# Kernel tuning notes

Hardware: AMD Instinct MI355X
Metric: run time of the kernel (lower is better)

## Reference

```python
import jax, jax.numpy as jnp
import numpy as np

FEATURE_DIM = 1024
HEAD_NUM = 16
HIDDEN_DIM = FEATURE_DIM // HEAD_NUM


def setup_inputs() -> dict:
    key = jax.random.key(0)
    ks = jax.random.split(key, 12)
    B, S, D = 4, 2048, FEATURE_DIM
    s = 1.0 / np.sqrt(D)
    inp = {
        "query": jax.random.normal(ks[0], (B, S, D), jnp.float32),
        "key": jax.random.normal(ks[1], (B, S, D), jnp.float32),
        "value": jax.random.normal(ks[2], (B, S, D), jnp.float32),
        "mask": jax.random.randint(ks[3], (B, 1, 1, S), 0, 2, jnp.int32),
        "Wq": jax.random.normal(ks[4], (D, D), jnp.float32) * s,
        "bq": jnp.zeros((D,), jnp.float32),
        "Wk": jax.random.normal(ks[5], (D, D), jnp.float32) * s,
        "bk": jnp.zeros((D,), jnp.float32),
        "Wv": jax.random.normal(ks[6], (D, D), jnp.float32) * s,
        "bv": jnp.zeros((D,), jnp.float32),
        "Wo": jax.random.normal(ks[7], (D, D), jnp.float32) * s,
        "bo": jnp.zeros((D,), jnp.float32),
    }
    return inp


def reference(query, key, value, mask, Wq, bq, Wk, bk, Wv, bv, Wo, bo):
    B, Sq, D = query.shape
    H, Hd = HEAD_NUM, HIDDEN_DIM
    scale = jnp.sqrt(jnp.asarray(Hd, query.dtype))

    def split_heads(x):
        b, s, _ = x.shape
        return x.reshape(b, s, H, Hd).transpose(0, 2, 1, 3)  # [B,H,S,Hd]

    Q = split_heads(query @ Wq.T + bq)
    K = split_heads(key @ Wk.T + bk)
    V = split_heads(value @ Wv.T + bv)

    scores = jnp.einsum("bhqd,bhkd->bhqk", Q, K) / scale
    scores = jnp.where(mask == 0, jnp.asarray(-1e10, scores.dtype), scores)
    attn = jax.nn.softmax(scores, axis=-1)  # dropout p=0 -> identity
    h = jnp.einsum("bhqk,bhkd->bhqd", attn, V)
    h = h.transpose(0, 2, 1, 3).reshape(B, Sq, D)
    return h @ Wo.T + bo
```

## Files before the change

kernel.cpp:

```cpp
#include <hip/hip_runtime.h>
#include <hip/hip_bf16.h>
#include <cstdint>
#include <cstddef>

#define D_MODEL 1024
#define SEQ     2048
#define BATCH   4
#define NHEAD   16
#define HD      64
#define MROWS   (BATCH * SEQ)

typedef __attribute__((ext_vector_type(8))) short  short8;
typedef __attribute__((ext_vector_type(4))) float  floatx4;
typedef __attribute__((ext_vector_type(4))) unsigned short ushort4v;
typedef unsigned short u16;

__device__ __forceinline__ u16 f2bf(float x) {
    __hip_bfloat16 h = __float2bfloat16(x);
    return *(u16*)&h;
}

__device__ __forceinline__ void async_copy16(const u16* g, u16* l) {
    __builtin_amdgcn_global_load_lds(
        (const __attribute__((address_space(1))) void*)g,
        (__attribute__((address_space(3))) void*)l, 16, 0, 0);
}

__device__ __forceinline__ void cvt8(const float* s, u16* d, size_t i) {
    const float4 a = *(const float4*)(s + i);
    const float4 b = *(const float4*)(s + i + 4);
    short8 o;
    o[0] = (short)f2bf(a.x); o[1] = (short)f2bf(a.y);
    o[2] = (short)f2bf(a.z); o[3] = (short)f2bf(a.w);
    o[4] = (short)f2bf(b.x); o[5] = (short)f2bf(b.y);
    o[6] = (short)f2bf(b.z); o[7] = (short)f2bf(b.w);
    *(short8*)(d + i) = o;
}

__global__ __launch_bounds__(256) void cvt7(
    const float* __restrict__ s0, const float* __restrict__ s1,
    const float* __restrict__ s2, const float* __restrict__ s3,
    const float* __restrict__ s4, const float* __restrict__ s5,
    const float* __restrict__ s6,
    u16* __restrict__ d0, u16* __restrict__ d1,
    u16* __restrict__ d2, u16* __restrict__ d3,
    u16* __restrict__ d4, u16* __restrict__ d5,
    u16* __restrict__ d6)
{
    const int y = blockIdx.y;
    const float* s;
    u16* d;
    size_t n;
    switch (y) {
        case 0: s = s0; d = d0; n = (size_t)D_MODEL * D_MODEL; break;
        case 1: s = s1; d = d1; n = (size_t)D_MODEL * D_MODEL; break;
        case 2: s = s2; d = d2; n = (size_t)D_MODEL * D_MODEL; break;
        case 3: s = s3; d = d3; n = (size_t)D_MODEL * D_MODEL; break;
        case 4: s = s4; d = d4; n = (size_t)MROWS * D_MODEL;   break;
        case 5: s = s5; d = d5; n = (size_t)MROWS * D_MODEL;   break;
        default: s = s6; d = d6; n = (size_t)MROWS * D_MODEL;  break;
    }
    const size_t i = ((size_t)blockIdx.x * 256 + threadIdx.x) * 8;
    if (i < n) cvt8(s, d, i);
}

__global__ __launch_bounds__(256) void gemm_qkv(
    const u16* __restrict__ Aq, const u16* __restrict__ Ak,
    const u16* __restrict__ Av,
    const u16* __restrict__ Wqp, const u16* __restrict__ Wkp,
    const u16* __restrict__ Wvp,
    const float* __restrict__ bqp, const float* __restrict__ bkp,
    const float* __restrict__ bvp,
    u16* __restrict__ oq, u16* __restrict__ ok, u16* __restrict__ ov)
{
    constexpr int K = D_MODEL;
    __shared__ __align__(16) u16 smem[32768];

    const int z = blockIdx.z;
    const u16*   A    = z == 0 ? Aq  : (z == 1 ? Ak  : Av);
    const u16*   W    = z == 0 ? Wqp : (z == 1 ? Wkp : Wvp);
    const float* bias = z == 0 ? bqp : (z == 1 ? bkp : bvp);
    u16*         out  = z == 0 ? oq  : (z == 1 ? ok  : ov);

    const int bm = blockIdx.x * 128;
    const int bn = blockIdx.y * 128;
    const int t  = threadIdx.x;
    const int w  = t >> 6;
    const int l  = t & 63;
    const int li = l & 15;
    const int quad = l >> 4;
    const int wm = (w & 1) * 64;
    const int wn = (w >> 1) * 64;
    const int lrow = l >> 3;
    const int lcol = (l & 7) * 8;

    const u16* Ag = A + (size_t)bm * K;
    const u16* Wg = W + (size_t)bn * K;

    floatx4 acc[4][4];
    #pragma unroll
    for (int mi = 0; mi < 4; mi++)
        #pragma unroll
        for (int ni = 0; ni < 4; ni++) acc[mi][ni] = (floatx4){0.f,0.f,0.f,0.f};

    #pragma unroll
    for (int j = 0; j < 4; j++) {
        const int r = w * 32 + j * 8;
        async_copy16(Ag + (size_t)(r + lrow) * K + lcol, smem + r * 64);
        async_copy16(Wg + (size_t)(r + lrow) * K + lcol, smem + 8192 + r * 64);
    }

    int cur = 0;
    for (int kt = 0; kt < K; kt += 64) {
        __syncthreads();

        if (kt + 64 < K) {
            u16* Asn = smem + (cur ^ 1) * 16384;
            u16* Wsn = Asn + 8192;
            #pragma unroll
            for (int j = 0; j < 4; j++) {
                const int r = w * 32 + j * 8;
                async_copy16(Ag + (size_t)(r + lrow) * K + kt + 64 + lcol, Asn + r * 64);
                async_copy16(Wg + (size_t)(r + lrow) * K + kt + 64 + lcol, Wsn + r * 64);
            }
        }

        const u16* Asc = smem + cur * 16384;
        const u16* Wsc = Asc + 8192;
        #pragma unroll
        for (int ks = 0; ks < 2; ks++) {
            short8 af[4], bf[4];
            #pragma unroll
            for (int i = 0; i < 4; i++) {
                af[i] = *(const short8*)&Asc[(wm + i * 16 + li) * 64 + ks * 32 + quad * 8];
                bf[i] = *(const short8*)&Wsc[(wn + i * 16 + li) * 64 + ks * 32 + quad * 8];
            }
            #pragma unroll
            for (int mi = 0; mi < 4; mi++)
                #pragma unroll
                for (int ni = 0; ni < 4; ni++)
                    acc[mi][ni] = __builtin_amdgcn_mfma_f32_16x16x32_bf16(
                        af[mi], bf[ni], acc[mi][ni], 0, 0, 0);
        }
        cur ^= 1;
    }

    if (z < 2) {
        #pragma unroll
        for (int mi = 0; mi < 4; mi++)
            #pragma unroll
            for (int ni = 0; ni < 4; ni++) {
                const int c  = bn + wn + ni * 16 + li;
                const int h  = c >> 6;
                const int hd = c & 63;
                const float bz = bias[c];
                #pragma unroll
                for (int reg = 0; reg < 4; reg++) {
                    const int r = bm + wm + mi * 16 + quad * 4 + reg;
                    const int b = r >> 11;
                    const int s = r & (SEQ - 1);
                    out[(((size_t)(b * NHEAD + h) * SEQ) + s) * HD + hd] = f2bf(acc[mi][ni][reg] + bz);
                }
            }
    } else {
        u16 (*Ct)[128] = (u16(*)[128])smem;
        __syncthreads();
        #pragma unroll
        for (int mi = 0; mi < 4; mi++)
            #pragma unroll
            for (int ni = 0; ni < 4; ni++) {
                const int cl = wn + ni * 16 + li;
                const float bz = bias[bn + cl];
                #pragma unroll
                for (int reg = 0; reg < 4; reg++) {
                    const int rl = wm + mi * 16 + quad * 4 + reg;
                    Ct[cl][rl] = f2bf(acc[mi][ni][reg] + bz);
                }
            }
        __syncthreads();
        const int cl   = t >> 1;
        const int half = t & 1;
        const int cg = bn + cl;
        const int h  = cg >> 6;
        const int hd = cg & 63;
        const int b  = bm >> 11;
        const int s0 = (bm & (SEQ - 1)) + half * 64;
        u16* dst = out + (((size_t)(b * NHEAD + h) * HD) + hd) * SEQ + s0;
        const short8* sp = (const short8*)&Ct[cl][half * 64];
        #pragma unroll
        for (int i = 0; i < 8; i++) ((short8*)dst)[i] = sp[i];
    }
}

__global__ __launch_bounds__(256) void gemm_out(
    const u16* __restrict__ A,
    const u16* __restrict__ W,
    const float* __restrict__ bias,
    float* __restrict__ out)
{
    constexpr int K = D_MODEL;
    __shared__ __align__(16) u16 smem[32768];

    const int bm = blockIdx.x * 128;
    const int bn = blockIdx.y * 128;
    const int t  = threadIdx.x;
    const int w  = t >> 6;
    const int l  = t & 63;
    const int li = l & 15;
    const int quad = l >> 4;
    const int wm = (w & 1) * 64;
    const int wn = (w >> 1) * 64;
    const int lrow = l >> 3;
    const int lcol = (l & 7) * 8;

    const u16* Ag = A + (size_t)bm * K;
    const u16* Wg = W + (size_t)bn * K;

    floatx4 acc[4][4];
    #pragma unroll
    for (int mi = 0; mi < 4; mi++)
        #pragma unroll
        for (int ni = 0; ni < 4; ni++) acc[mi][ni] = (floatx4){0.f,0.f,0.f,0.f};

    #pragma unroll
    for (int j = 0; j < 4; j++) {
        const int r = w * 32 + j * 8;
        async_copy16(Ag + (size_t)(r + lrow) * K + lcol, smem + r * 64);
        async_copy16(Wg + (size_t)(r + lrow) * K + lcol, smem + 8192 + r * 64);
    }

    int cur = 0;
    for (int kt = 0; kt < K; kt += 64) {
        __syncthreads();

        if (kt + 64 < K) {
            u16* Asn = smem + (cur ^ 1) * 16384;
            u16* Wsn = Asn + 8192;
            #pragma unroll
            for (int j = 0; j < 4; j++) {
                const int r = w * 32 + j * 8;
                async_copy16(Ag + (size_t)(r + lrow) * K + kt + 64 + lcol, Asn + r * 64);
                async_copy16(Wg + (size_t)(r + lrow) * K + kt + 64 + lcol, Wsn + r * 64);
            }
        }

        const u16* Asc = smem + cur * 16384;
        const u16* Wsc = Asc + 8192;
        #pragma unroll
        for (int ks = 0; ks < 2; ks++) {
            short8 af[4], bf[4];
            #pragma unroll
            for (int i = 0; i < 4; i++) {
                af[i] = *(const short8*)&Asc[(wm + i * 16 + li) * 64 + ks * 32 + quad * 8];
                bf[i] = *(const short8*)&Wsc[(wn + i * 16 + li) * 64 + ks * 32 + quad * 8];
            }
            #pragma unroll
            for (int mi = 0; mi < 4; mi++)
                #pragma unroll
                for (int ni = 0; ni < 4; ni++)
                    acc[mi][ni] = __builtin_amdgcn_mfma_f32_16x16x32_bf16(
                        af[mi], bf[ni], acc[mi][ni], 0, 0, 0);
        }
        cur ^= 1;
    }

    #pragma unroll
    for (int mi = 0; mi < 4; mi++)
        #pragma unroll
        for (int ni = 0; ni < 4; ni++) {
            const int c = bn + wn + ni * 16 + li;
            const float bz = bias[c];
            #pragma unroll
            for (int reg = 0; reg < 4; reg++) {
                const int r = bm + wm + mi * 16 + quad * 4 + reg;
                out[(size_t)r * D_MODEL + c] = acc[mi][ni][reg] + bz;
            }
        }
}

#define LOG2E   1.44269504088896340736f
#define CSCALE  (0.125f * LOG2E)

__global__ __launch_bounds__(256, 4) void attn_mfma(
    const u16* __restrict__ Q,
    const u16* __restrict__ K,
    const u16* __restrict__ Vt,
    const int* __restrict__ mask,
    u16* __restrict__ H)
{
    __shared__ __align__(16) u16 Ks[64 * 64];
    __shared__ __align__(16) u16 Vs[64 * 64];
    __shared__ __align__(16) u16 Ps[4][32][72];
    __shared__ __align__(16) float mc[64];

    const int bh  = blockIdx.y;
    const int b   = bh >> 4;
    const int h   = bh & 15;
    const int q0  = blockIdx.x * 128;
    const int t   = threadIdx.x;
    const int w   = t >> 6;
    const int l   = t & 63;
    const int li  = l & 15;
    const int quad  = l >> 4;
    const int lrow8 = l >> 3;
    const int gch   = (l & 7) ^ lrow8;
    const int swz   = li & 7;

    short8 qf[2][2];
    #pragma unroll
    for (int qb = 0; qb < 2; qb++) {
        const u16* Qrow = Q + ((size_t)bh * SEQ + q0 + w * 32 + qb * 16 + li) * HD;
        qf[qb][0] = *(const short8*)(Qrow + quad * 8);
        qf[qb][1] = *(const short8*)(Qrow + 32 + quad * 8);
    }

    const u16* Kbh = K  + (size_t)bh * SEQ * HD;
    const u16* Vbh = Vt + (size_t)bh * HD * SEQ;
    const int* mg  = mask + (size_t)b * SEQ;

    floatx4 oacc[4][2];
    #pragma unroll
    for (int hm = 0; hm < 4; hm++)
        #pragma unroll
        for (int qb = 0; qb < 2; qb++) oacc[hm][qb] = (floatx4){0.f,0.f,0.f,0.f};
    float rs[2] = {0.f, 0.f};

    #pragma unroll
    for (int j = 0; j < 2; j++) {
        const int rb = w * 16 + j * 8;
        async_copy16(Kbh + (size_t)(rb + lrow8) * HD + gch * 8, &Ks[rb * 64]);
    }
    if (t < 64) mc[t] = (mg[t] != 0) ? -16.0f : -1.0e9f;

    for (int kt = 0; kt < SEQ; kt += 64) {
        __syncthreads();

        #pragma unroll
        for (int j = 0; j < 2; j++) {
            const int rb = w * 16 + j * 8;
            async_copy16(Vbh + (size_t)(rb + lrow8) * SEQ + kt + gch * 8,
                         &Vs[rb * 64]);
        }

        #pragma unroll
        for (int kb = 0; kb < 4; kb++) {
            floatx4 s0 = (floatx4){0.f,0.f,0.f,0.f};
            floatx4 s1 = (floatx4){0.f,0.f,0.f,0.f};
            #pragma unroll
            for (int ks = 0; ks < 2; ks++) {
                const short8 kf = *(const short8*)
                    &Ks[(kb * 16 + li) * 64 + ((ks * 4 + quad) ^ swz) * 8];
                __builtin_amdgcn_s_setprio(1);
                s0 = __builtin_amdgcn_mfma_f32_16x16x32_bf16(kf, qf[0][ks], s0, 0, 0, 0);
                s1 = __builtin_amdgcn_mfma_f32_16x16x32_bf16(kf, qf[1][ks], s1, 0, 0, 0);
                __builtin_amdgcn_s_setprio(0);
            }
            const float4 m4 = *(const float4*)&mc[kb * 16 + quad * 4];
            {
                const float p0 = __builtin_amdgcn_exp2f(fmaf(s0[0], CSCALE, m4.x));
                const float p1 = __builtin_amdgcn_exp2f(fmaf(s0[1], CSCALE, m4.y));
                const float p2 = __builtin_amdgcn_exp2f(fmaf(s0[2], CSCALE, m4.z));
                const float p3 = __builtin_amdgcn_exp2f(fmaf(s0[3], CSCALE, m4.w));
                rs[0] += (p0 + p1) + (p2 + p3);
                ushort4v pk;
                pk[0] = f2bf(p0); pk[1] = f2bf(p1);
                pk[2] = f2bf(p2); pk[3] = f2bf(p3);
                *(ushort4v*)&Ps[w][li][kb * 16 + quad * 4] = pk;
            }
            {
                const float p0 = __builtin_amdgcn_exp2f(fmaf(s1[0], CSCALE, m4.x));
                const float p1 = __builtin_amdgcn_exp2f(fmaf(s1[1], CSCALE, m4.y));
                const float p2 = __builtin_amdgcn_exp2f(fmaf(s1[2], CSCALE, m4.z));
                const float p3 = __builtin_amdgcn_exp2f(fmaf(s1[3], CSCALE, m4.w));
                rs[1] += (p0 + p1) + (p2 + p3);
                ushort4v pk;
                pk[0] = f2bf(p0); pk[1] = f2bf(p1);
                pk[2] = f2bf(p2); pk[3] = f2bf(p3);
                *(ushort4v*)&Ps[w][16 + li][kb * 16 + quad * 4] = pk;
            }
        }

        __syncthreads();

        if (kt + 64 < SEQ) {
            #pragma unroll
            for (int j = 0; j < 2; j++) {
                const int rb = w * 16 + j * 8;
                async_copy16(Kbh + (size_t)(kt + 64 + rb + lrow8) * HD + gch * 8,
                             &Ks[rb * 64]);
            }
            if (t < 64) mc[t] = (mg[kt + 64 + t] != 0) ? -16.0f : -1.0e9f;
        }

        #pragma unroll
        for (int ks = 0; ks < 2; ks++) {
            short8 pf[2];
            #pragma unroll
            for (int qb = 0; qb < 2; qb++)
                pf[qb] = *(const short8*)&Ps[w][qb * 16 + li][ks * 32 + quad * 8];
            __builtin_amdgcn_s_setprio(1);
            #pragma unroll
            for (int hm = 0; hm < 4; hm++) {
                const short8 vf = *(const short8*)&Vs[(hm * 16 + li) * 64 + ((ks * 4 + quad) ^ swz) * 8];
                #pragma unroll
                for (int qb = 0; qb < 2; qb++)
                    oacc[hm][qb] = __builtin_amdgcn_mfma_f32_16x16x32_bf16(
                        vf, pf[qb], oacc[hm][qb], 0, 0, 0);
            }
            __builtin_amdgcn_s_setprio(0);
        }
    }

    float linv[2];
    #pragma unroll
    for (int qb = 0; qb < 2; qb++) {
        float v = rs[qb];
        v += __shfl_xor(v, 16, 64);
        v += __shfl_xor(v, 32, 64);
        linv[qb] = 1.0f / v;
    }
    #pragma unroll
    for (int qb = 0; qb < 2; qb++) {
        const size_t row = (size_t)b * SEQ + q0 + w * 32 + qb * 16 + li;
        #pragma unroll
        for (int hm = 0; hm < 4; hm++) {
            ushort4v o;
            #pragma unroll
            for (int reg = 0; reg < 4; reg++)
                o[reg] = f2bf(oacc[hm][qb][reg] * linv[qb]);
            *(ushort4v*)&H[row * D_MODEL + h * 64 + hm * 16 + quad * 4] = o;
        }
    }
}

extern "C" void kernel_launch(void* const* d_in, const int* in_sizes, int n_in,
                              void* d_out, int out_size, void* d_ws, size_t ws_size,
                              hipStream_t stream)
{
    const float* query = (const float*)d_in[0];
    const float* key_  = (const float*)d_in[1];
    const float* value = (const float*)d_in[2];
    const int*   mask  = (const int*)  d_in[3];
    const float* Wq = (const float*)d_in[4];
    const float* bq = (const float*)d_in[5];
    const float* Wk = (const float*)d_in[6];
    const float* bk = (const float*)d_in[7];
    const float* Wv = (const float*)d_in[8];
    const float* bv = (const float*)d_in[9];
    const float* Wo = (const float*)d_in[10];
    const float* bo = (const float*)d_in[11];
    float* out = (float*)d_out;

    const size_t per = (size_t)BATCH * NHEAD * SEQ * HD;
    const size_t wsz = (size_t)D_MODEL * D_MODEL;
    u16* Qb  = (u16*)d_ws;
    u16* Kb  = Qb  + per;
    u16* Vtb = Kb  + per;
    u16* Wqb = Vtb + per;
    u16* Wkb = Wqb + wsz;
    u16* Wvb = Wkb + wsz;
    u16* Wob = Wvb + wsz;
    u16* Aqb = Wob + wsz;
    u16* Akb = Aqb + per;
    u16* Avb = Akb + per;
    u16* Hb  = Aqb;

    cvt7<<<dim3((per / 8 + 255) / 256, 7), 256, 0, stream>>>(
        Wq, Wk, Wv, Wo, query, key_, value,
        Wqb, Wkb, Wvb, Wob, Aqb, Akb, Avb);

    gemm_qkv<<<dim3(MROWS / 128, D_MODEL / 128, 3), 256, 0, stream>>>(
        Aqb, Akb, Avb, Wqb, Wkb, Wvb, bq, bk, bv, Qb, Kb, Vtb);

    attn_mfma<<<dim3(SEQ / 128, BATCH * NHEAD), 256, 0, stream>>>(
        Qb, Kb, Vtb, mask, Hb);

    gemm_out<<<dim3(MROWS / 128, D_MODEL / 128), 256, 0, stream>>>(
        Hb, Wob, bo, out);
}
```

Measured before the change: 344.5 us.

## Fuse fp32-to-bf16 activation conversion into QKV GEMM A-tile loading

The separate conversion pass over the query, key and value activations is removed. The QKV GEMM now loads fp32 A tiles into registers, converts them to bf16 and stores them to shared memory after the MFMA work of each k-step, while the weights are still converted by a smaller 4-way kernel. This removes a full read/write round trip of the three activation tensors, in exchange for more register pressure and synchronous conversion work inside the GEMM. Each A tile is read once per N-block as fp32, which is twice the bytes of the bf16 version.

```diff
diff --git a/kernel.cpp b/kernel.cpp
--- a/kernel.cpp
+++ b/kernel.cpp
@@ -37,36 +37,22 @@
     *(short8*)(d + i) = o;
 }
 
-__global__ __launch_bounds__(256) void cvt7(
+__global__ __launch_bounds__(256) void cvt4(
     const float* __restrict__ s0, const float* __restrict__ s1,
     const float* __restrict__ s2, const float* __restrict__ s3,
-    const float* __restrict__ s4, const float* __restrict__ s5,
-    const float* __restrict__ s6,
     u16* __restrict__ d0, u16* __restrict__ d1,
-    u16* __restrict__ d2, u16* __restrict__ d3,
-    u16* __restrict__ d4, u16* __restrict__ d5,
-    u16* __restrict__ d6)
+    u16* __restrict__ d2, u16* __restrict__ d3)
 {
-    const int y = blockIdx.y;
-    const float* s;
-    u16* d;
-    size_t n;
-    switch (y) {
-        case 0: s = s0; d = d0; n = (size_t)D_MODEL * D_MODEL; break;
-        case 1: s = s1; d = d1; n = (size_t)D_MODEL * D_MODEL; break;
-        case 2: s = s2; d = d2; n = (size_t)D_MODEL * D_MODEL; break;
-        case 3: s = s3; d = d3; n = (size_t)D_MODEL * D_MODEL; break;
-        case 4: s = s4; d = d4; n = (size_t)MROWS * D_MODEL;   break;
-        case 5: s = s5; d = d5; n = (size_t)MROWS * D_MODEL;   break;
-        default: s = s6; d = d6; n = (size_t)MROWS * D_MODEL;  break;
-    }
-    const size_t i = ((size_t)blockIdx.x * 256 + threadIdx.x) * 8;
-    if (i < n) cvt8(s, d, i);
+    const float* s = blockIdx.y == 0 ? s0 : (blockIdx.y == 1 ? s1 :
+                     (blockIdx.y == 2 ? s2 : s3));
+    u16*         d = blockIdx.y == 0 ? d0 : (blockIdx.y == 1 ? d1 :
+                     (blockIdx.y == 2 ? d2 : d3));
+    cvt8(s, d, ((size_t)blockIdx.x * 256 + threadIdx.x) * 8);
 }
 
 __global__ __launch_bounds__(256) void gemm_qkv(
-    const u16* __restrict__ Aq, const u16* __restrict__ Ak,
-    const u16* __restrict__ Av,
+    const float* __restrict__ Aq, const float* __restrict__ Ak,
+    const float* __restrict__ Av,
     const u16* __restrict__ Wqp, const u16* __restrict__ Wkp,
     const u16* __restrict__ Wvp,
     const float* __restrict__ bqp, const float* __restrict__ bkp,
@@ -77,7 +63,7 @@
     __shared__ __align__(16) u16 smem[32768];
 
     const int z = blockIdx.z;
-    const u16*   A    = z == 0 ? Aq  : (z == 1 ? Ak  : Av);
+    const float* A    = z == 0 ? Aq  : (z == 1 ? Ak  : Av);
     const u16*   W    = z == 0 ? Wqp : (z == 1 ? Wkp : Wvp);
     const float* bias = z == 0 ? bqp : (z == 1 ? bkp : bvp);
     u16*         out  = z == 0 ? oq  : (z == 1 ? ok  : ov);
@@ -93,9 +79,13 @@
     const int wn = (w >> 1) * 64;
     const int lrow = l >> 3;
     const int lcol = (l & 7) * 8;
-
-    const u16* Ag = A + (size_t)bm * K;
-    const u16* Wg = W + (size_t)bn * K;
+    const int srow = w * 32 + (l >> 3);
+    const int lc8  = (l & 7) * 8;
+
+    const float* Ab = A + (size_t)bm * K;
+    const u16*   Wg = W + (size_t)bn * K;
+
+    float4 pa[4][2];
 
     floatx4 acc[4][4];
     #pragma unroll
@@ -103,24 +93,43 @@
         #pragma unroll
         for (int ni = 0; ni < 4; ni++) acc[mi][ni] = (floatx4){0.f,0.f,0.f,0.f};
 
+    #pragma unroll
+    for (int j = 0; j < 4; j++) {
+        const float* ap = Ab + (size_t)(srow + j * 8) * K + lc8;
+        pa[j][0] = *(const float4*)ap;
+        pa[j][1] = *(const float4*)(ap + 4);
+    }
     #pragma unroll
     for (int j = 0; j < 4; j++) {
         const int r = w * 32 + j * 8;
-        async_copy16(Ag + (size_t)(r + lrow) * K + lcol, smem + r * 64);
         async_copy16(Wg + (size_t)(r + lrow) * K + lcol, smem + 8192 + r * 64);
+    }
+    #pragma unroll
+    for (int j = 0; j < 4; j++) {
+        short8 av;
+        av[0] = (short)f2bf(pa[j][0].x); av[1] = (short)f2bf(pa[j][0].y);
+        av[2] = (short)f2bf(pa[j][0].z); av[3] = (short)f2bf(pa[j][0].w);
+        av[4] = (short)f2bf(pa[j][1].x); av[5] = (short)f2bf(pa[j][1].y);
+        av[6] = (short)f2bf(pa[j][1].z); av[7] = (short)f2bf(pa[j][1].w);
+        *(short8*)&smem[(srow + j * 8) * 64 + lc8] = av;
     }
 
     int cur = 0;
     for (int kt = 0; kt < K; kt += 64) {
         __syncthreads();
 
-        if (kt + 64 < K) {
-            u16* Asn = smem + (cur ^ 1) * 16384;
-            u16* Wsn = Asn + 8192;
+        const bool pf = (kt + 64 < K);
+        if (pf) {
+            #pragma unroll
+            for (int j = 0; j < 4; j++) {
+                const float* ap = Ab + (size_t)(srow + j * 8) * K + kt + 64 + lc8;
+                pa[j][0] = *(const float4*)ap;
+                pa[j][1] = *(const float4*)(ap + 4);
+            }
+            u16* Wsn = smem + (cur ^ 1) * 16384 + 8192;
             #pragma unroll
             for (int j = 0; j < 4; j++) {
                 const int r = w * 32 + j * 8;
-                async_copy16(Ag + (size_t)(r + lrow) * K + kt + 64 + lcol, Asn + r * 64);
                 async_copy16(Wg + (size_t)(r + lrow) * K + kt + 64 + lcol, Wsn + r * 64);
             }
         }
@@ -141,6 +150,19 @@
                 for (int ni = 0; ni < 4; ni++)
                     acc[mi][ni] = __builtin_amdgcn_mfma_f32_16x16x32_bf16(
                         af[mi], bf[ni], acc[mi][ni], 0, 0, 0);
+        }
+
+        if (pf) {
+            u16* Asn = smem + (cur ^ 1) * 16384;
+            #pragma unroll
+            for (int j = 0; j < 4; j++) {
+                short8 av;
+                av[0] = (short)f2bf(pa[j][0].x); av[1] = (short)f2bf(pa[j][0].y);
+                av[2] = (short)f2bf(pa[j][0].z); av[3] = (short)f2bf(pa[j][0].w);
+                av[4] = (short)f2bf(pa[j][1].x); av[5] = (short)f2bf(pa[j][1].y);
+                av[6] = (short)f2bf(pa[j][1].z); av[7] = (short)f2bf(pa[j][1].w);
+                *(short8*)&Asn[(srow + j * 8) * 64 + lc8] = av;
+            }
         }
         cur ^= 1;
     }
@@ -460,17 +482,13 @@
     u16* Wkb = Wqb + wsz;
     u16* Wvb = Wkb + wsz;
     u16* Wob = Wvb + wsz;
-    u16* Aqb = Wob + wsz;
-    u16* Akb = Aqb + per;
-    u16* Avb = Akb + per;
-    u16* Hb  = Aqb;
-
-    cvt7<<<dim3((per / 8 + 255) / 256, 7), 256, 0, stream>>>(
-        Wq, Wk, Wv, Wo, query, key_, value,
-        Wqb, Wkb, Wvb, Wob, Aqb, Akb, Avb);
+    u16* Hb  = Wob + wsz;
+
+    cvt4<<<dim3(wsz / 2048, 4), 256, 0, stream>>>(Wq, Wk, Wv, Wo,
+                                                  Wqb, Wkb, Wvb, Wob);
 
     gemm_qkv<<<dim3(MROWS / 128, D_MODEL / 128, 3), 256, 0, stream>>>(
-        Aqb, Akb, Avb, Wqb, Wkb, Wvb, bq, bk, bv, Qb, Kb, Vtb);
+        query, key_, value, Wqb, Wkb, Wvb, bq, bk, bv, Qb, Kb, Vtb);
 
     attn_mfma<<<dim3(SEQ / 128, BATCH * NHEAD), 256, 0, stream>>>(
         Qb, Kb, Vtb, mask, Hb);
```

Result: no change. 340.7 us (-1.1%).
